# Kernel tuning notes

Measured on AMD Instinct MI355X. Metric: run time of the kernel, lower is better.

Reference implementation:

```python
import jax, jax.numpy as jnp
import numpy as np

B, T_IN, T_OUT, D, M, N = 4, 10, 5, 5, 96, 96
H1 = 64      # hidden dim of deep ConvLSTM layers
ATTN = 32    # attention bottleneck channels
SEL = 0      # selected_dim


def _conv(x, w, b):
    # SAME conv, NCHW / OIHW
    p = (w.shape[-1] - 1) // 2
    y = jax.lax.conv_general_dilated(x, w, (1, 1), [(p, p), (p, p)],
                                     dimension_numbers=('NCHW', 'OIHW', 'NCHW'))
    return y + b[None, :, None, None]


def _cell(xt, h, c, w, b):
    # standard ConvLSTM cell (no peephole): conv over concat(x, h) -> i,f,o,g
    z = _conv(jnp.concatenate([xt, h], axis=1), w, b)
    i, f, o, g = jnp.split(z, 4, axis=1)
    c = jax.nn.sigmoid(f) * c + jax.nn.sigmoid(i) * jnp.tanh(g)
    h = jax.nn.sigmoid(o) * jnp.tanh(c)
    return h, c


def setup_inputs() -> dict:
    key = jax.random.key(0)
    ks = jax.random.split(key, 12)
    w = lambda k, s: jax.random.normal(k, s, jnp.float32) * 0.05
    z = lambda n: jnp.zeros((n,), jnp.float32)
    return {
        'x': jax.random.normal(ks[0], (B, T_IN, D, M, N), jnp.float32),
        # encoder ConvLSTM cells: hidden dims [1, H1, H1]
        'enc_w0': w(ks[1], (4 * 1, D + 1, 3, 3)), 'enc_b0': z(4 * 1),
        'enc_w1': w(ks[2], (4 * H1, 1 + H1, 3, 3)), 'enc_b1': z(4 * H1),
        'enc_w2': w(ks[3], (4 * H1, H1 + H1, 3, 3)), 'enc_b2': z(4 * H1),
        # decoder ConvLSTM cells: hidden dims [H1, H1, 1]
        'dec_w0': w(ks[4], (4 * H1, 1 + H1, 3, 3)), 'dec_b0': z(4 * H1),
        'dec_w1': w(ks[5], (4 * H1, H1 + H1, 3, 3)), 'dec_b1': z(4 * H1),
        'dec_w2': w(ks[6], (4 * 1, H1 + 1, 3, 3)), 'dec_b2': z(4 * 1),
        # input attention (DA-RNN style with convs): e_k = v(tanh(Wi*x_k + Wh*[h;c]))
        'attn_wi': w(ks[7], (ATTN, T_IN, 3, 3)), 'attn_bi': z(ATTN),
        'attn_wh': w(ks[8], (ATTN, 2, 3, 3)), 'attn_bh': z(ATTN),
        'attn_wv': w(ks[9], (1, ATTN, 3, 3)), 'attn_bv': z(1),
        # temporal_cnn: Conv2d(1 + window_in, 1, kernel_size=1) + ReLU
        'tcnn_w': w(ks[10], (1, T_IN + 1, 1, 1)), 'tcnn_b': z(1),
    }


def reference(x, enc_w0, enc_b0, enc_w1, enc_b1, enc_w2, enc_b2,
              dec_w0, dec_b0, dec_w1, dec_b1, dec_w2, dec_b2,
              attn_wi, attn_bi, attn_wh, attn_bh, attn_wv, attn_bv,
              tcnn_w, tcnn_b):
    b = x.shape[0]

    def attn_reweight(xs, h, c):
        # xs: (b, t, d, m, n); hidden term shared across the d channels
        hid_e = _conv(jnp.concatenate([h, c], axis=1), attn_wh, attn_bh)
        def per_k(xk):  # (b, t, m, n): time-as-channels
            e = jnp.tanh(_conv(xk, attn_wi, attn_bi) + hid_e)
            return _conv(e, attn_wv, attn_bv)[:, 0]  # (b, m, n)
        alpha = jax.vmap(per_k, in_axes=2, out_axes=1)(xs)  # (b, d, m, n)
        ea = jnp.exp(alpha)
        return xs * (ea / jnp.max(ea))[:, None]  # global-max normalization

    def run_layer(xs, h, c, w, bb):
        def step(carry, xt):
            hh, cc = _cell(xt, carry[0], carry[1], w, bb)
            return (hh, cc), hh
        (h, c), hs = jax.lax.scan(step, (h, c), jnp.swapaxes(xs, 0, 1))
        return jnp.swapaxes(hs, 0, 1), (h, c)

    # ---------- encoder ----------
    h0 = jnp.zeros((b, 1, M, N), x.dtype); c0 = jnp.zeros_like(h0)
    def enc0_step(carry, t):
        xs, h, c = carry
        xs = attn_reweight(xs, h, c)  # re-weight whole sequence each step
        xt = jax.lax.dynamic_index_in_dim(xs, t, axis=1, keepdims=False)
        h, c = _cell(xt, h, c, enc_w0, enc_b0)
        return (xs, h, c), h
    (_, h0, c0), hs0 = jax.lax.scan(enc0_step, (x, h0, c0), jnp.arange(T_IN))
    out0 = jnp.swapaxes(hs0, 0, 1)  # (b, T_IN, 1, m, n)

    h1 = jnp.zeros((b, H1, M, N), x.dtype); c1 = jnp.zeros_like(h1)
    out1, (h1, c1) = run_layer(out0, h1, c1, enc_w1, enc_b1)
    h2 = jnp.zeros((b, H1, M, N), x.dtype); c2 = jnp.zeros_like(h2)
    out2, (h2, c2) = run_layer(out1, h2, c2, enc_w2, enc_b2)

    # ---------- decoder (encoder states reversed) ----------
    dec_in = jnp.zeros((b, T_OUT, 1, M, N), x.dtype)
    d0, _ = run_layer(dec_in, h2, c2, dec_w0, dec_b0)
    d1, _ = run_layer(d0, h1, c1, dec_w1, dec_b1)

    y_prev = x[:, :, SEL]  # (b, T_IN, m, n): selected variable, time-as-channels
    def dec2_step(carry, xt):
        h, c, yp = carry
        h, c = _cell(xt, h, c, dec_w2, dec_b2)          # (b, 1, m, n)
        ycat = jnp.concatenate([yp, h], axis=1)         # (b, T_IN+1, m, n)
        h = jax.nn.relu(_conv(ycat, tcnn_w, tcnn_b))    # temporal 1x1 CNN readout
        return (h, c, ycat[:, 1:]), h
    _, hs = jax.lax.scan(dec2_step, (h0, c0, y_prev), jnp.swapaxes(d1, 0, 1))
    return jnp.swapaxes(hs, 0, 1)  # (b, T_OUT, 1, m, n)
```

## Files before the change

kernel.cpp:

```cpp
#include <hip/hip_runtime.h>


#define PIX  9216
#define NB   4
#define TIN  10
#define TOUT 5
#define ND   5
#define HID  64

typedef __attribute__((ext_vector_type(8))) short bf16x8;
typedef __attribute__((ext_vector_type(4))) float f32x4;

__device__ __forceinline__ float sigmf_(float x) { return 1.0f / (1.0f + __expf(-x)); }
__device__ __forceinline__ float tanhf_(float x) { return 1.0f - 2.0f / (__expf(2.0f * x) + 1.0f); }
__device__ __forceinline__ unsigned short f2bf(float f) {
    unsigned u = __float_as_uint(f);
    unsigned r = u + 0x7FFFu + ((u >> 16) & 1u);
    return (unsigned short)(r >> 16);
}
__device__ __forceinline__ float bf2f(unsigned short u) {
    return __uint_as_float(((unsigned)u) << 16);
}
__device__ __forceinline__ unsigned fmap_(float f) {
    unsigned u = __float_as_uint(f);
    return (u & 0x80000000u) ? ~u : (u | 0x80000000u);
}
__device__ __forceinline__ float funmap_(unsigned v) {
    return __uint_as_float((v & 0x80000000u) ? (v ^ 0x80000000u) : ~v);
}
__device__ __forceinline__ void gload_lds16(const void* g, void* l) {
    __builtin_amdgcn_global_load_lds(
        (const __attribute__((address_space(1))) void*)g,
        (__attribute__((address_space(3))) void*)l, 16, 0, 0);
}

template <int NCH>
__device__ __forceinline__ void
cell64_body(char* smem, int bid,
            const unsigned short* __restrict__ inP,
            const unsigned short* __restrict__ wP,
            const float* __restrict__ bias,
            const float* cprev, float* cout,
            const float* __restrict__ zeropg,
            unsigned short* __restrict__ d1, int d1_coff, int d1_ncg,
            unsigned short* __restrict__ d2, int d2_coff, int d2_ncg)
{
    const int lane = threadIdx.x;
    const int wv   = threadIdx.y;
    const int tid  = wv * 64 + lane;
    const int rid = (bid & 7) * 48 + (bid >> 3);
    const int y = rid % 96, b = rid / 96;
    const int l15 = lane & 15, l4 = lane >> 4;
    const int NCG = NCH * 4;

    const int scg  = tid & 3;
    const int spr0 = tid >> 2;

    auto stage = [&](char* buf, int cc) {
#pragma unroll
        for (int i = 0; i < 5; ++i) {
            int pr = spr0 + i * 64;
            int r = pr / 98;
            int p = pr - r * 98;
            int gy = y - 1 + r, gx = p - 1;
            const void* g = (const void*)zeropg;
            if (pr < 294 && (unsigned)gy < 96u && (unsigned)gx < 96u) {
                int cg = scg ^ ((p >> 1) & 3);
                g = (const void*)(inP + (((size_t)(b * NCG + cc * 4 + cg) * 9216
                                          + gy * 96 + gx) << 3));
            }
            gload_lds16(g, buf + i * 4096 + wv * 1024);
        }
    };

    f32x4 acc[4][6] = {};
    bf16x8 af[3][4];

#pragma unroll
    for (int t0 = 0; t0 < 2; ++t0)
#pragma unroll
        for (int g = 0; g < 4; ++g)
            af[t0][g] = *(const bf16x8*)(wP
                + ((size_t)(t0 * NCH + 0) * 256 + g * 64 + wv * 16 + l15) * 32 + l4 * 8);

    stage(smem, 0);
    __syncthreads();
#pragma unroll
    for (int cc = 0; cc < NCH; ++cc) {
        if (cc + 1 < NCH) stage(smem + ((cc + 1) & 1) * 20480, cc + 1);
        const char* buf = smem + (cc & 1) * 20480;
#pragma unroll
        for (int tap = 0; tap < 9; ++tap) {
            const int T = cc * 9 + tap;
            const int Tp = T + 2;
            if (Tp < NCH * 9) {
                const int cc2 = Tp / 9, tap2 = Tp % 9;
#pragma unroll
                for (int g = 0; g < 4; ++g)
                    af[Tp % 3][g] = *(const bf16x8*)(wP
                        + ((size_t)(tap2 * NCH + cc2) * 256 + g * 64 + wv * 16 + l15) * 32 + l4 * 8);
            }
            const int ky = tap / 3, kx = tap % 3;
            bf16x8 bk[6];
#pragma unroll
            for (int k = 0; k < 6; ++k) {
                int p = k * 16 + kx + l15;
                int slot = l4 ^ ((p >> 1) & 3);
                bk[k] = *(const bf16x8*)(buf + (ky * 98 + p) * 64 + slot * 16);
            }
            __builtin_amdgcn_s_setprio(1);
#pragma unroll
            for (int g = 0; g < 4; ++g)
#pragma unroll
                for (int k = 0; k < 6; ++k)
                    acc[g][k] = __builtin_amdgcn_mfma_f32_16x16x32_bf16(
                        af[T % 3][g], bk[k], acc[g][k], 0, 0, 0);
            __builtin_amdgcn_s_setprio(0);
        }
        if (cc + 1 < NCH) __syncthreads();
    }

#pragma unroll
    for (int r = 0; r < 4; ++r) {
        int hc = wv * 16 + l4 * 4 + r;
        float bi = bias[hc], bff = bias[64 + hc];
        float bo = bias[128 + hc], bg = bias[192 + hc];
#pragma unroll
        for (int k = 0; k < 6; ++k) {
            int px = k * 16 + l15;
            int gpix = y * 96 + px;
            float ii = sigmf_(acc[0][k][r] + bi);
            float ff = sigmf_(acc[1][k][r] + bff);
            float oo = sigmf_(acc[2][k][r] + bo);
            float gg = tanhf_(acc[3][k][r] + bg);
            int cidx = (b * HID + hc) * 9216 + gpix;
            float cn = ff * cprev[cidx] + ii * gg;
            cout[cidx] = cn;
            unsigned short hb = f2bf(oo * tanhf_(cn));
            int ch1 = d1_coff + hc;
            d1[((size_t)(b * d1_ncg + (ch1 >> 3)) * 9216 + gpix) * 8 + (ch1 & 7)] = hb;
            if (d2) {
                int ch2 = d2_coff + hc;
                d2[((size_t)(b * d2_ncg + (ch2 >> 3)) * 9216 + gpix) * 8 + (ch2 & 7)] = hb;
            }
        }
    }
}

__device__ __forceinline__ void
attnE_body(char* smem, int aid,
           const unsigned short* __restrict__ xsp, const unsigned short* __restrict__ wiP,
           const float* __restrict__ h0, const float* __restrict__ c0,
           const float* __restrict__ wh, const float* __restrict__ bh,
           const float* __restrict__ bi, unsigned short* __restrict__ eP)
{
    float* heS = (float*)smem;
    const int lane = threadIdx.x, wvid = threadIdx.y;
    const int tile = aid % 36, k = (aid / 36) % 5, bb = aid / 180;
    const int l15 = lane & 15, l4 = lane >> 4;
    const int tid = wvid * 64 + lane;

    {
        int p = tile * 256 + tid;
        int y = p / 96, x = p - y * 96;
        float hv9[9], cv9[9];
        const float* hp = h0 + bb * PIX;
        const float* cp = c0 + bb * PIX;
#pragma unroll
        for (int t9 = 0; t9 < 9; ++t9) {
            int gy = y + t9 / 3 - 1, gx = x + t9 % 3 - 1;
            bool ok = (unsigned)gy < 96u && (unsigned)gx < 96u;
            hv9[t9] = ok ? hp[gy * 96 + gx] : 0.0f;
            cv9[t9] = ok ? cp[gy * 96 + gx] : 0.0f;
        }
#pragma unroll
        for (int ch = 0; ch < 32; ++ch) {
            float a = bi[ch] + bh[ch];
#pragma unroll
            for (int t9 = 0; t9 < 9; ++t9) {
                a = fmaf(wh[(ch * 2 + 0) * 9 + t9], hv9[t9], a);
                a = fmaf(wh[(ch * 2 + 1) * 9 + t9], cv9[t9], a);
            }
            heS[tid * 33 + ch] = a;
        }
    }

    bf16x8 af[5][2];
#pragma unroll
    for (int j = 0; j < 5; ++j)
#pragma unroll
        for (int m = 0; m < 2; ++m)
            af[j][m] = *(const bf16x8*)(wiP + ((size_t)(j * 32 + m * 16 + l15)) * 32 + l4 * 8);

    const unsigned short* xb = xsp + (size_t)(bb * ND + k) * PIX * 16;
    const int p0 = tile * 256 + wvid * 64;

    f32x4 acc[4][2] = {};
#pragma unroll
    for (int nf = 0; nf < 4; ++nf) {
        int p = p0 + nf * 16 + l15;
        int y = p / 96, x = p - y * 96;
#pragma unroll
        for (int j = 0; j < 5; ++j) {
            int tp = 2 * j + (l4 >> 1);
            bf16x8 bk = { 0, 0, 0, 0, 0, 0, 0, 0 };
            if (tp < 9) {
                int gy = y + tp / 3 - 1, gx = x + tp % 3 - 1;
                if ((unsigned)gy < 96u && (unsigned)gx < 96u)
                    bk = *(const bf16x8*)(xb + ((size_t)(gy * 96 + gx)) * 16 + (l4 & 1) * 8);
            }
            acc[nf][0] = __builtin_amdgcn_mfma_f32_16x16x32_bf16(af[j][0], bk, acc[nf][0], 0, 0, 0);
            acc[nf][1] = __builtin_amdgcn_mfma_f32_16x16x32_bf16(af[j][1], bk, acc[nf][1], 0, 0, 0);
        }
    }

    __syncthreads();

#pragma unroll
    for (int nf = 0; nf < 4; ++nf) {
        int p = p0 + nf * 16 + l15;
        int pl = wvid * 64 + nf * 16 + l15;
        const float* hrow = &heS[pl * 33];
#pragma unroll
        for (int m = 0; m < 2; ++m) {
            ushort4 o;
            o.x = f2bf(tanhf_(acc[nf][m][0] + hrow[m * 16 + l4 * 4 + 0]));
            o.y = f2bf(tanhf_(acc[nf][m][1] + hrow[m * 16 + l4 * 4 + 1]));
            o.z = f2bf(tanhf_(acc[nf][m][2] + hrow[m * 16 + l4 * 4 + 2]));
            o.w = f2bf(tanhf_(acc[nf][m][3] + hrow[m * 16 + l4 * 4 + 3]));
            *(ushort4*)(eP + ((size_t)(bb * ND + k) * PIX + p) * 32 + m * 16 + l4 * 4) = o;
        }
    }
}

__device__ __forceinline__ void
alpha_body(char* smem, int aid,
           const unsigned short* __restrict__ eP, const float* __restrict__ wvv,
           const float* __restrict__ bv, float* __restrict__ alpha,
           unsigned* __restrict__ msl)
{
    const int tid = threadIdx.y * 64 + threadIdx.x;
    const int tile = aid % 36, k = (aid / 36) % 5, bb = aid / 180;
    int p = tile * 256 + tid;
    int y = p / 96, x = p - y * 96;
    const unsigned short* eb = eP + (size_t)(bb * ND + k) * PIX * 32;
    float acc = bv[0];
#pragma unroll
    for (int ky = 0; ky < 3; ++ky) {
        int gy = y + ky - 1;
        if ((unsigned)gy >= 96u) continue;
#pragma unroll
        for (int kx = 0; kx < 3; ++kx) {
            int gx = x + kx - 1;
            if ((unsigned)gx >= 96u) continue;
            int tap = ky * 3 + kx;
            const unsigned short* ee = eb + ((size_t)(gy * 96 + gx)) * 32;
#pragma unroll
            for (int cg = 0; cg < 4; ++cg) {
                bf16x8 ev = *(const bf16x8*)(ee + cg * 8);
#pragma unroll
                for (int jj = 0; jj < 8; ++jj)
                    acc = fmaf(wvv[(cg * 8 + jj) * 9 + tap], bf2f((unsigned short)ev[jj]), acc);
            }
        }
    }
    alpha[(size_t)(bb * ND + k) * PIX + p] = acc;

    float* s = (float*)smem;
    s[tid] = acc;
    __syncthreads();
    for (int st = 128; st > 0; st >>= 1) {
        if (tid < st) s[tid] = fmaxf(s[tid], s[tid + st]);
        __syncthreads();
    }
    if (tid == 0) atomicMax(msl, fmap_(s[0]));
}

__device__ __forceinline__ void
dec2_body(int did,
          const unsigned short* __restrict__ inP, int ncg, int cgbase,
          const float* __restrict__ hprev, const float* cprev,
          const unsigned short* __restrict__ wm, const float* __restrict__ w2,
          const float* __restrict__ bias,
          const float* __restrict__ tw, const float* __restrict__ tb,
          const float* __restrict__ yprev,
          float* __restrict__ ynext, float* __restrict__ hcarry,
          float* __restrict__ outp, float* cout)
{
    const int wv = threadIdx.y, lane = threadIdx.x;
    const int l15 = lane & 15, l4 = lane >> 4;
    const int bx = did % 144, b = did / 144;
    const int p0 = (bx * 4 + wv) * 16;
    const int y = p0 / 96, xbase = p0 - y * 96;
    const int x = xbase + l15;

    f32x4 acc = {0.f, 0.f, 0.f, 0.f};
#pragma unroll
    for (int ky = 0; ky < 3; ++ky) {
        int gy = y + ky - 1;
        bool oky = (unsigned)gy < 96u;
#pragma unroll
        for (int kx = 0; kx < 3; ++kx) {
            const int tap = ky * 3 + kx;
            int gx = x + kx - 1;
            bool ok = oky && ((unsigned)gx < 96u);
#pragma unroll
            for (int cc = 0; cc < 2; ++cc) {
                bf16x8 a = *(const bf16x8*)(wm + ((size_t)(tap * 2 + cc) * 16 + l15) * 32 + l4 * 8);
                bf16x8 bk = { 0, 0, 0, 0, 0, 0, 0, 0 };
                if (ok)
                    bk = *(const bf16x8*)(inP + ((size_t)(b * ncg + cgbase + cc * 4 + l4) * 9216
                                                 + gy * 96 + gx) * 8);
                acc = __builtin_amdgcn_mfma_f32_16x16x32_bf16(a, bk, acc, 0, 0, 0);
            }
        }
    }

    if (l4 == 0) {
        int px = p0 + l15;
        float aI = acc[0] + bias[0];
        float aF = acc[1] + bias[1];
        float aO = acc[2] + bias[2];
        float aG = acc[3] + bias[3];
        const float* hp = hprev + b * PIX;
#pragma unroll
        for (int ky = 0; ky < 3; ++ky) {
            int gy = y + ky - 1;
            if ((unsigned)gy >= 96u) continue;
#pragma unroll
            for (int kx = 0; kx < 3; ++kx) {
                int gx = x + kx - 1;
                if ((unsigned)gx >= 96u) continue;
                int tap = ky * 3 + kx;
                float hv = hp[gy * 96 + gx];
                aI = fmaf(w2[(0 * 65 + 64) * 9 + tap], hv, aI);
                aF = fmaf(w2[(1 * 65 + 64) * 9 + tap], hv, aF);
                aO = fmaf(w2[(2 * 65 + 64) * 9 + tap], hv, aO);
                aG = fmaf(w2[(3 * 65 + 64) * 9 + tap], hv, aG);
            }
        }
        int idx = b * PIX + px;
        float cn = sigmf_(aF) * cprev[idx] + sigmf_(aI) * tanhf_(aG);
        cout[idx] = cn;
        float h = sigmf_(aO) * tanhf_(cn);

        float a2 = tb[0];
#pragma unroll
        for (int c2 = 0; c2 < TIN; ++c2)
            a2 = fmaf(tw[c2], yprev[(size_t)(b * TIN + c2) * PIX + px], a2);
        a2 = fmaf(tw[TIN], h, a2);
        float o = fmaxf(a2, 0.0f);
        outp[(size_t)b * TOUT * PIX + px] = o;
#pragma unroll
        for (int c2 = 0; c2 < TIN - 1; ++c2)
            ynext[(size_t)(b * TIN + c2) * PIX + px] = yprev[(size_t)(b * TIN + c2 + 1) * PIX + px];
        ynext[(size_t)(b * TIN + 9) * PIX + px] = h;
        hcarry[idx] = o;
    }
}

template <int NCH, bool ATTN>
__global__ void __launch_bounds__(256, 2)
mk_cell_attnE(const unsigned short* __restrict__ inP, const unsigned short* __restrict__ wP,
              const float* __restrict__ bias, const float* cprev, float* cout,
              const float* __restrict__ zeropg,
              unsigned short* __restrict__ d1, int d1_coff, int d1_ncg,
              unsigned short* __restrict__ d2, int d2_coff, int d2_ncg,
              const unsigned short* __restrict__ xsp, const unsigned short* __restrict__ wiP,
              const float* __restrict__ h0, const float* __restrict__ c0,
              const float* __restrict__ wh, const float* __restrict__ bh,
              const float* __restrict__ bi, unsigned short* __restrict__ eP)
{
    __shared__ __align__(16) char smem[40960];
    if (blockIdx.x < 384)
        cell64_body<NCH>(smem, blockIdx.x, inP, wP, bias, cprev, cout, zeropg,
                         d1, d1_coff, d1_ncg, d2, d2_coff, d2_ncg);
    else if (ATTN)
        attnE_body(smem, blockIdx.x - 384, xsp, wiP, h0, c0, wh, bh, bi, eP);
}

template <int NCH, bool ATTN>
__global__ void __launch_bounds__(256, 2)
mk_cell_alpha(const unsigned short* __restrict__ inP, const unsigned short* __restrict__ wP,
              const float* __restrict__ bias, const float* cprev, float* cout,
              const float* __restrict__ zeropg,
              unsigned short* __restrict__ d1, int d1_coff, int d1_ncg,
              unsigned short* __restrict__ d2, int d2_coff, int d2_ncg,
              const unsigned short* __restrict__ eP, const float* __restrict__ wvv,
              const float* __restrict__ bv, float* __restrict__ alpha,
              unsigned* __restrict__ msl)
{
    __shared__ __align__(16) char smem[40960];
    if (blockIdx.x < 384)
        cell64_body<NCH>(smem, blockIdx.x, inP, wP, bias, cprev, cout, zeropg,
                         d1, d1_coff, d1_ncg, d2, d2_coff, d2_ncg);
    else if (ATTN)
        alpha_body(smem, blockIdx.x - 384, eP, wvv, bv, alpha, msl);
}

__global__ void __launch_bounds__(256)
mk_scale_small5(const float* __restrict__ xs_cur, float* __restrict__ xs_nxt,
                unsigned short* __restrict__ xsp,
                const float* __restrict__ alpha, const unsigned* __restrict__ msl,
                int ts,
                const float* __restrict__ h0in, const float* cprev,
                const float* __restrict__ w, const float* __restrict__ bias,
                float* __restrict__ h0out, float* cout,
                unsigned short* __restrict__ pk, int ncg)
{
    __shared__ float z[4][64];
    const int bid = blockIdx.x;
    const float mval = funmap_(msl[0]);
    if (bid < 720) {
        int idx = bid * 256 + threadIdx.x;
        int p = idx % PIX;
        int q = idx / PIX;
        int d = q % ND, bb = q / ND;
        float wgt = __expf(alpha[idx] - mval);
        unsigned short tmp[16];
#pragma unroll
        for (int t = 0; t < TIN; ++t) {
            size_t xi = ((size_t)(bb * TIN + t) * ND + d) * PIX + p;
            float v = xs_cur[xi] * wgt;
            xs_nxt[xi] = v;
            tmp[t] = f2bf(v);
        }
#pragma unroll
        for (int t = TIN; t < 16; ++t) tmp[t] = 0;
        uint4* dst = (uint4*)(xsp + (size_t)idx * 16);
        dst[0] = *(uint4*)&tmp[0];
        dst[1] = *(uint4*)&tmp[8];
    } else {
        int bid2 = bid - 720;
        int bx = bid2 % 144, bb = bid2 / 144;
        const int pxl = threadIdx.x & 63, gate = threadIdx.x >> 6;
        const int p = bx * 64 + pxl;
        const int y = p / 96, x = p - y * 96;
        float acc = bias[gate];
#pragma unroll
        for (int cin = 0; cin < 6; ++cin) {
            const float* wp = w + (gate * 6 + cin) * 9;
#pragma unroll
            for (int ky = 0; ky < 3; ++ky) {
                int gy = y + ky - 1;
                if ((unsigned)gy >= 96u) continue;
#pragma unroll
                for (int kx = 0; kx < 3; ++kx) {
                    int gx = x + kx - 1;
                    if ((unsigned)gx >= 96u) continue;
                    int np = gy * 96 + gx;
                    float v;
                    if (cin < 5) {
                        float raw = xs_cur[((size_t)(bb * TIN + ts) * ND + cin) * PIX + np];
                        v = raw * __expf(alpha[(size_t)(bb * ND + cin) * PIX + np] - mval);
                    } else {
                        v = h0in[bb * PIX + np];
                    }
                    acc = fmaf(wp[ky * 3 + kx], v, acc);
                }
            }
        }
        z[gate][pxl] = acc;
        __syncthreads();
        if (threadIdx.x < 64) {
            int pp = bx * 64 + threadIdx.x;
            int idx = bb * PIX + pp;
            float cn = sigmf_(z[1][threadIdx.x]) * cprev[idx]
                     + sigmf_(z[0][threadIdx.x]) * tanhf_(z[3][threadIdx.x]);
            cout[idx] = cn;
            float h = sigmf_(z[2][threadIdx.x]) * tanhf_(cn);
            h0out[idx] = h;
            pk[((size_t)(bb * ncg) * 9216 + pp) * 8] = f2bf(h);
        }
    }
}

template <bool HAS0, bool HAS2>
__global__ void __launch_bounds__(256, 2)
mk_dec(const unsigned short* __restrict__ d1in, const unsigned short* __restrict__ wpd1,
       const float* __restrict__ b1, float* c1, unsigned short* __restrict__ d1out,
       const float* __restrict__ zeropg,
       const unsigned short* __restrict__ d0in, const unsigned short* __restrict__ wpd0,
       const float* __restrict__ b0, float* c2, unsigned short* __restrict__ d0out,
       unsigned short* __restrict__ d1next,
       const unsigned short* __restrict__ d2in,
       const float* __restrict__ hprev, float* c0,
       const unsigned short* __restrict__ wd2m, const float* __restrict__ w2,
       const float* __restrict__ b2,
       const float* __restrict__ tw, const float* __restrict__ tb,
       const float* __restrict__ yprev, float* __restrict__ ynext,
       float* __restrict__ hcarry, float* __restrict__ outp)
{
    __shared__ __align__(16) char smem[40960];
    if (blockIdx.x < 384) {
        cell64_body<4>(smem, blockIdx.x, d1in, wpd1, b1, c1, c1, zeropg,
                       d1out, 64, 16, nullptr, 0, 0);
    } else if (blockIdx.x < 768) {
        if (HAS0)
            cell64_body<2>(smem, blockIdx.x - 384, d0in, wpd0, b0, c2, c2, zeropg,
                           d0out, 0, 8, d1next, 0, 16);
    } else {
        if (HAS2)
            dec2_body(blockIdx.x - 768, d2in, 16, 8, hprev, c0, wd2m, w2, b2,
                      tw, tb, yprev, ynext, hcarry, outp, c0);
    }
}

template <int NCH>
__global__ void __launch_bounds__(256, 2)
cell_k(const unsigned short* __restrict__ inP, const unsigned short* __restrict__ wP,
       const float* __restrict__ bias, const float* cprev, float* cout,
       const float* __restrict__ zeropg,
       unsigned short* __restrict__ d1, int d1_coff, int d1_ncg,
       unsigned short* __restrict__ d2, int d2_coff, int d2_ncg)
{
    __shared__ __align__(16) char smem[40960];
    cell64_body<NCH>(smem, blockIdx.x, inP, wP, bias, cprev, cout, zeropg,
                     d1, d1_coff, d1_ncg, d2, d2_coff, d2_ncg);
}

__global__ void __launch_bounds__(256)
dec2_k(const unsigned short* __restrict__ d2in, const float* __restrict__ hprev,
       float* c0, const unsigned short* __restrict__ wd2m, const float* __restrict__ w2,
       const float* __restrict__ b2, const float* __restrict__ tw, const float* __restrict__ tb,
       const float* __restrict__ yprev, float* __restrict__ ynext,
       float* __restrict__ hcarry, float* __restrict__ outp)
{
    dec2_body(blockIdx.x, d2in, 16, 8, hprev, c0, wd2m, w2, b2,
              tw, tb, yprev, ynext, hcarry, outp, c0);
}

__global__ void __launch_bounds__(256)
attn_e_k(const unsigned short* __restrict__ xsp, const unsigned short* __restrict__ wiP,
         const float* __restrict__ h0, const float* __restrict__ c0,
         const float* __restrict__ wh, const float* __restrict__ bh,
         const float* __restrict__ bi, unsigned short* __restrict__ eP)
{
    __shared__ __align__(16) char smem[33792];
    attnE_body(smem, blockIdx.x, xsp, wiP, h0, c0, wh, bh, bi, eP);
}

__global__ void __launch_bounds__(256)
alpha_k(const unsigned short* __restrict__ eP, const float* __restrict__ wvv,
        const float* __restrict__ bv, float* __restrict__ alpha, unsigned* __restrict__ msl)
{
    __shared__ __align__(16) char smem[1024];
    alpha_body(smem, blockIdx.x, eP, wvv, bv, alpha, msl);
}

__global__ void __launch_bounds__(256)
prep_kernel(const float* __restrict__ enc_w1, const float* __restrict__ enc_w2,
            const float* __restrict__ dec_w0, const float* __restrict__ dec_w1,
            const float* __restrict__ dec_w2, const float* __restrict__ attn_wi,
            const float* __restrict__ x,
            unsigned short* __restrict__ wpe1, unsigned short* __restrict__ wpe2,
            unsigned short* __restrict__ wpd0, unsigned short* __restrict__ wpd1,
            unsigned short* __restrict__ wd2m, unsigned short* __restrict__ wiP,
            unsigned short* __restrict__ xsp, float* __restrict__ yp)
{
    int gid = blockIdx.x;
    auto wpack = [&](const float* w, unsigned short* wp, int WCIN, int NCH,
                     int coff, int climit, int base) {
        int idx = (gid - base) * 256 + threadIdx.x;
        if (idx >= 9 * NCH * 256 * 32) return;
        int k = idx & 31;
        int ocp = (idx >> 5) & 255;
        int rest = idx >> 13;
        int cc = rest % NCH, tap = rest / NCH;
        int hc = ocp >> 2, gate = ocp & 3;
        int c = cc * 32 + k;
        float v = 0.0f;
        if (c < climit) v = w[((gate * 64 + hc) * WCIN + (c + coff)) * 9 + tap];
        wp[idx] = f2bf(v);
    };
    if (gid < 864) { wpack(enc_w1, wpe1, 65, 3, 0, 65, 0); return; }
    if (gid < 2016) { wpack(enc_w2, wpe2, 128, 4, 0, 128, 864); return; }
    if (gid < 2592) { wpack(dec_w0, wpd0, 65, 2, 1, 64, 2016); return; }
    if (gid < 3744) { wpack(dec_w1, wpd1, 128, 4, 0, 128, 2592); return; }
    if (gid < 3780) {
        int idx = (gid - 3744) * 256 + threadIdx.x;
        if (idx < 9 * 2 * 16 * 32) {
            int k = idx & 31;
            int oc = (idx >> 5) & 15;
            int cc = (idx >> 9) & 1;
            int tap = idx >> 10;
            float v = 0.0f;
            if (oc < 4) v = dec_w2[(oc * 65 + cc * 32 + k) * 9 + tap];
            wd2m[idx] = f2bf(v);
        }
        return;
    }
    if (gid < 3800) {
        int idx = (gid - 3780) * 256 + threadIdx.x;
        if (idx < 5120) {
            int kl = idx & 31, oc = (idx >> 5) & 31, j = idx >> 10;
            int tappos = kl >> 4, ch = kl & 15;
            int tap = 2 * j + tappos;
            float v = 0.0f;
            if (tap < 9 && ch < 10) v = attn_wi[(oc * TIN + ch) * 9 + tap];
            wiP[idx] = f2bf(v);
        }
        return;
    }
    if (gid < 4520) {
        int idx = (gid - 3800) * 256 + threadIdx.x;
        int p = idx % PIX;
        int q = idx / PIX;
        int d = q % ND, bb = q / ND;
        unsigned short tmp[16];
#pragma unroll
        for (int t = 0; t < TIN; ++t)
            tmp[t] = f2bf(x[((size_t)(bb * TIN + t) * ND + d) * PIX + p]);
#pragma unroll
        for (int t = TIN; t < 16; ++t) tmp[t] = 0;
        uint4* dst = (uint4*)(xsp + (size_t)idx * 16);
        dst[0] = *(uint4*)&tmp[0];
        dst[1] = *(uint4*)&tmp[8];
        return;
    }
    {
        int idx = (gid - 4520) * 256 + threadIdx.x;
        int p = idx % PIX;
        int q = idx / PIX;
        yp[idx] = x[(size_t)(q * ND + 0) * PIX + p];
    }
}

extern "C" void kernel_launch(void* const* d_in, const int* in_sizes, int n_in,
                              void* d_out, int out_size, void* d_ws, size_t ws_size,
                              hipStream_t stream)
{
    const float* x       = (const float*)d_in[0];
    const float* enc_w0  = (const float*)d_in[1];
    const float* enc_b0  = (const float*)d_in[2];
    const float* enc_w1  = (const float*)d_in[3];
    const float* enc_b1  = (const float*)d_in[4];
    const float* enc_w2  = (const float*)d_in[5];
    const float* enc_b2  = (const float*)d_in[6];
    const float* dec_w0  = (const float*)d_in[7];
    const float* dec_b0  = (const float*)d_in[8];
    const float* dec_w1  = (const float*)d_in[9];
    const float* dec_b1  = (const float*)d_in[10];
    const float* dec_w2  = (const float*)d_in[11];
    const float* dec_b2  = (const float*)d_in[12];
    const float* attn_wi = (const float*)d_in[13];
    const float* attn_bi = (const float*)d_in[14];
    const float* attn_wh = (const float*)d_in[15];
    const float* attn_bh = (const float*)d_in[16];
    const float* attn_wv = (const float*)d_in[17];
    const float* attn_bv = (const float*)d_in[18];
    const float* tcnn_w  = (const float*)d_in[19];
    const float* tcnn_b  = (const float*)d_in[20];
    float* out = (float*)d_out;

    char* cur = (char*)d_ws;
    auto alloc = [&](size_t bytes) { char* p = cur; cur += (bytes + 255) & ~(size_t)255; return p; };
    float* xsA  = (float*)alloc((size_t)NB * TIN * ND * PIX * 4);
    float* xsB  = (float*)alloc((size_t)NB * TIN * ND * PIX * 4);
    float* alp  = (float*)alloc((size_t)NB * ND * PIX * 4);
    float* ypa  = (float*)alloc((size_t)NB * TIN * PIX * 4);
    float* ypb  = (float*)alloc((size_t)NB * TIN * PIX * 4);
    unsigned short* wpe1 = (unsigned short*)alloc((size_t)9 * 3 * 256 * 32 * 2);
    unsigned short* wpe2 = (unsigned short*)alloc((size_t)9 * 4 * 256 * 32 * 2);
    unsigned short* wpd0 = (unsigned short*)alloc((size_t)9 * 2 * 256 * 32 * 2);
    unsigned short* wpd1 = (unsigned short*)alloc((size_t)9 * 4 * 256 * 32 * 2);
    unsigned short* wd2m = (unsigned short*)alloc((size_t)9 * 2 * 16 * 32 * 2);
    unsigned short* xsp  = (unsigned short*)alloc((size_t)NB * ND * PIX * 16 * 2);
    unsigned short* wiP  = (unsigned short*)alloc(5120 * 2);
    unsigned short* eP   = (unsigned short*)alloc((size_t)NB * ND * PIX * 32 * 2);
    char* zbeg = cur;
    float* h0a  = (float*)alloc(NB * PIX * 4);
    float* h0b  = (float*)alloc(NB * PIX * 4);
    float* c0   = (float*)alloc(NB * PIX * 4);
    float* c1   = (float*)alloc((size_t)NB * HID * PIX * 4);
    float* c2   = (float*)alloc((size_t)NB * HID * PIX * 4);
    const size_t IN1_B = (size_t)NB * 12 * PIX * 8 * 2;
    const size_t IN2_B = (size_t)NB * 16 * PIX * 8 * 2;
    unsigned short* In1a = (unsigned short*)alloc(IN1_B);
    unsigned short* In1b = (unsigned short*)alloc(IN1_B);
    unsigned short* In2a = (unsigned short*)alloc(IN2_B);
    unsigned short* In2b = (unsigned short*)alloc(IN2_B);
    unsigned* mslot = (unsigned*)alloc(256);
    float* zeropg = (float*)alloc(256);
    char* zend = cur;

    hipMemcpyAsync(xsA, x, (size_t)NB * TIN * ND * PIX * 4, hipMemcpyDeviceToDevice, stream);
    hipMemsetAsync(zbeg, 0, (size_t)(zend - zbeg), stream);
    prep_kernel<<<dim3(5960), 256, 0, stream>>>(enc_w1, enc_w2, dec_w0, dec_w1, dec_w2,
                                                attn_wi, x, wpe1, wpe2, wpd0, wpd1,
                                                wd2m, wiP, xsp, ypa);

    dim3 blk(64, 4);
    float *h0 = h0a, *h0n = h0b;
    float *xc = xsA, *xn = xsB;
    unsigned short *i1c = In1a, *i1n = In1b, *i2c = In2a, *i2n = In2b;

    attn_e_k<<<dim3(720), blk, 0, stream>>>(xsp, wiP, h0, c0, attn_wh, attn_bh, attn_bi, eP);
    alpha_k<<<dim3(720), blk, 0, stream>>>(eP, attn_wv, attn_bv, alp, mslot + 0);
    mk_scale_small5<<<dim3(1296), 256, 0, stream>>>(xc, xn, xsp, alp, mslot + 0, 0,
                                                    h0, c0, enc_w0, enc_b0, h0n, c0, i1c, 12);
    { float* tmp = h0; h0 = h0n; h0n = tmp; }
    { float* tmp = xc; xc = xn; xn = tmp; }

    for (int t = 0; t < TIN; ++t) {
        const bool hn = (t < TIN - 1);
        unsigned short* e1d1 = hn ? i1n : In2a;
        int e1o = hn ? 1 : 64;
        int e1n = hn ? 12 : 16;
        unsigned short* e2d1 = hn ? i2n : In1a;
        int e2o = hn ? 64 : 0;
        int e2n = hn ? 16 : 8;
        int grid = 384 + (hn ? 720 : 0);

        if (hn)
            mk_cell_attnE<3, true><<<dim3(grid), blk, 0, stream>>>(
                i1c, wpe1, enc_b1, c1, c1, zeropg, e1d1, e1o, e1n, i2c, 0, 16,
                xsp, wiP, h0, c0, attn_wh, attn_bh, attn_bi, eP);
        else
            mk_cell_attnE<3, false><<<dim3(grid), blk, 0, stream>>>(
                i1c, wpe1, enc_b1, c1, c1, zeropg, e1d1, e1o, e1n, i2c, 0, 16,
                xsp, wiP, h0, c0, attn_wh, attn_bh, attn_bi, eP);

        if (hn)
            mk_cell_alpha<4, true><<<dim3(grid), blk, 0, stream>>>(
                i2c, wpe2, enc_b2, c2, c2, zeropg, e2d1, e2o, e2n, nullptr, 0, 0,
                eP, attn_wv, attn_bv, alp, mslot + t + 1);
        else
            mk_cell_alpha<4, false><<<dim3(grid), blk, 0, stream>>>(
                i2c, wpe2, enc_b2, c2, c2, zeropg, e2d1, e2o, e2n, nullptr, 0, 0,
                eP, attn_wv, attn_bv, alp, mslot + t + 1);

        if (hn) {
            mk_scale_small5<<<dim3(1296), 256, 0, stream>>>(xc, xn, xsp, alp, mslot + t + 1,
                                                            t + 1, h0, c0, enc_w0, enc_b0,
                                                            h0n, c0, i1n, 12);
            { float* tmp = h0; h0 = h0n; h0n = tmp; }
            { float* tmp = xc; xc = xn; xn = tmp; }
        }
        { unsigned short* tmp = i1c; i1c = i1n; i1n = tmp; }
        { unsigned short* tmp = i2c; i2c = i2n; i2n = tmp; }
    }

    float *hc = h0, *hcn = h0n;
    cell_k<2><<<dim3(384), blk, 0, stream>>>(In1a, wpd0, dec_b0, c2, c2, zeropg,
                                             In1b, 0, 8, In2a, 0, 16);
    mk_dec<true, false><<<dim3(768), blk, 0, stream>>>(
        In2a, wpd1, dec_b1, c1, In2b, zeropg,
        In1b, wpd0, dec_b0, c2, In1a, In2b,
        nullptr, nullptr, nullptr, nullptr, nullptr, nullptr, nullptr, nullptr,
        nullptr, nullptr, nullptr, nullptr);
    mk_dec<true, true><<<dim3(1344), blk, 0, stream>>>(
        In2b, wpd1, dec_b1, c1, In2a, zeropg,
        In1a, wpd0, dec_b0, c2, In1b, In2a,
        In2b, hc, c0, wd2m, dec_w2, dec_b2, tcnn_w, tcnn_b,
        ypa, ypb, hcn, out + 0 * PIX);
    mk_dec<true, true><<<dim3(1344), blk, 0, stream>>>(
        In2a, wpd1, dec_b1, c1, In2b, zeropg,
        In1b, wpd0, dec_b0, c2, In1a, In2b,
        In2a, hcn, c0, wd2m, dec_w2, dec_b2, tcnn_w, tcnn_b,
        ypb, ypa, hc, out + 1 * PIX);
    mk_dec<true, true><<<dim3(1344), blk, 0, stream>>>(
        In2b, wpd1, dec_b1, c1, In2a, zeropg,
        In1a, wpd0, dec_b0, c2, In1b, In2a,
        In2b, hc, c0, wd2m, dec_w2, dec_b2, tcnn_w, tcnn_b,
        ypa, ypb, hcn, out + 2 * PIX);
    mk_dec<false, true><<<dim3(1344), blk, 0, stream>>>(
        In2a, wpd1, dec_b1, c1, In2b, zeropg,
        nullptr, nullptr, nullptr, nullptr, nullptr, nullptr,
        In2a, hcn, c0, wd2m, dec_w2, dec_b2, tcnn_w, tcnn_b,
        ypb, ypa, hc, out + 3 * PIX);
    dec2_k<<<dim3(576), blk, 0, stream>>>(In2b, hc, c0, wd2m, dec_w2, dec_b2,
                                          tcnn_w, tcnn_b, ypa, ypb, hcn, out + 4 * PIX);
}
```

Baseline: 1.270 ms.

## Split encoder layer-1 single input channel into separate direct-gather MFMA pass

The encoder layer-1 cell previously packed its one input channel plus 64 hidden channels into 3 channel chunks (65 channels padded to 96). The input channel is now handled by a dedicated MFMA pass that gathers the 9 conv taps of the fp32 h0 map directly from global memory, using a separately packed weight slice. This lets the main loop run over only 2 chunks, and the scale kernel no longer writes h0 into the packed bf16 input buffer. It removes a mostly-padding chunk of LDS staging and MFMA work, at the cost of uncoalesced scalar global gathers and extra registers in the cell kernel.

```diff
diff --git a/kernel.cpp b/kernel.cpp
--- a/kernel.cpp
+++ b/kernel.cpp
@@ -34,7 +34,7 @@
         (__attribute__((address_space(3))) void*)l, 16, 0, 0);
 }
 
-template <int NCH>
+template <int NCH, bool XCONV>
 __device__ __forceinline__ void
 cell64_body(char* smem, int bid,
             const unsigned short* __restrict__ inP,
@@ -43,7 +43,8 @@
             const float* cprev, float* cout,
             const float* __restrict__ zeropg,
             unsigned short* __restrict__ d1, int d1_coff, int d1_ncg,
-            unsigned short* __restrict__ d2, int d2_coff, int d2_ncg)
+            unsigned short* __restrict__ d2, int d2_coff, int d2_ncg,
+            const float* __restrict__ xim, const unsigned short* __restrict__ wxP)
 {
     const int lane = threadIdx.x;
     const int wv   = threadIdx.y;
@@ -118,6 +119,33 @@
             __builtin_amdgcn_s_setprio(0);
         }
         if (cc + 1 < NCH) __syncthreads();
+    }
+
+    if (XCONV) {
+        bf16x8 afx[4];
+#pragma unroll
+        for (int g = 0; g < 4; ++g)
+            afx[g] = *(const bf16x8*)(wxP
+                + ((size_t)(g * 64 + wv * 16 + l15)) * 32 + l4 * 8);
+        const float* xb = xim + b * PIX;
+#pragma unroll
+        for (int k = 0; k < 6; ++k) {
+            int p = k * 16 + l15;
+            bf16x8 bx = { 0, 0, 0, 0, 0, 0, 0, 0 };
+#pragma unroll
+            for (int j = 0; j < 8; ++j) {
+                int tap = l4 * 8 + j;
+                if (tap < 9) {
+                    int gy = y + tap / 3 - 1, gx = p + tap % 3 - 1;
+                    if ((unsigned)gy < 96u && (unsigned)gx < 96u)
+                        bx[j] = (short)f2bf(xb[gy * 96 + gx]);
+                }
+            }
+#pragma unroll
+            for (int g = 0; g < 4; ++g)
+                acc[g][k] = __builtin_amdgcn_mfma_f32_16x16x32_bf16(
+                    afx[g], bx, acc[g][k], 0, 0, 0);
+        }
     }
 
 #pragma unroll
@@ -359,13 +387,14 @@
     }
 }
 
-template <int NCH, bool ATTN>
+template <int NCH, bool XCONV, bool ATTN>
 __global__ void __launch_bounds__(256, 2)
 mk_cell_attnE(const unsigned short* __restrict__ inP, const unsigned short* __restrict__ wP,
               const float* __restrict__ bias, const float* cprev, float* cout,
               const float* __restrict__ zeropg,
               unsigned short* __restrict__ d1, int d1_coff, int d1_ncg,
               unsigned short* __restrict__ d2, int d2_coff, int d2_ncg,
+              const float* __restrict__ xim, const unsigned short* __restrict__ wxP,
               const unsigned short* __restrict__ xsp, const unsigned short* __restrict__ wiP,
               const float* __restrict__ h0, const float* __restrict__ c0,
               const float* __restrict__ wh, const float* __restrict__ bh,
@@ -373,8 +402,8 @@
 {
     __shared__ __align__(16) char smem[40960];
     if (blockIdx.x < 384)
-        cell64_body<NCH>(smem, blockIdx.x, inP, wP, bias, cprev, cout, zeropg,
-                         d1, d1_coff, d1_ncg, d2, d2_coff, d2_ncg);
+        cell64_body<NCH, XCONV>(smem, blockIdx.x, inP, wP, bias, cprev, cout, zeropg,
+                                d1, d1_coff, d1_ncg, d2, d2_coff, d2_ncg, xim, wxP);
     else if (ATTN)
         attnE_body(smem, blockIdx.x - 384, xsp, wiP, h0, c0, wh, bh, bi, eP);
 }
@@ -392,8 +421,8 @@
 {
     __shared__ __align__(16) char smem[40960];
     if (blockIdx.x < 384)
-        cell64_body<NCH>(smem, blockIdx.x, inP, wP, bias, cprev, cout, zeropg,
-                         d1, d1_coff, d1_ncg, d2, d2_coff, d2_ncg);
+        cell64_body<NCH, false>(smem, blockIdx.x, inP, wP, bias, cprev, cout, zeropg,
+                                d1, d1_coff, d1_ncg, d2, d2_coff, d2_ncg, nullptr, nullptr);
     else if (ATTN)
         alpha_body(smem, blockIdx.x - 384, eP, wvv, bv, alpha, msl);
 }
@@ -405,8 +434,7 @@
                 int ts,
                 const float* __restrict__ h0in, const float* cprev,
                 const float* __restrict__ w, const float* __restrict__ bias,
-                float* __restrict__ h0out, float* cout,
-                unsigned short* __restrict__ pk, int ncg)
+                float* __restrict__ h0out, float* cout)
 {
     __shared__ float z[4][64];
     const int bid = blockIdx.x;
@@ -468,9 +496,7 @@
             float cn = sigmf_(z[1][threadIdx.x]) * cprev[idx]
                      + sigmf_(z[0][threadIdx.x]) * tanhf_(z[3][threadIdx.x]);
             cout[idx] = cn;
-            float h = sigmf_(z[2][threadIdx.x]) * tanhf_(cn);
-            h0out[idx] = h;
-            pk[((size_t)(bb * ncg) * 9216 + pp) * 8] = f2bf(h);
+            h0out[idx] = sigmf_(z[2][threadIdx.x]) * tanhf_(cn);
         }
     }
 }
@@ -493,12 +519,12 @@
 {
     __shared__ __align__(16) char smem[40960];
     if (blockIdx.x < 384) {
-        cell64_body<4>(smem, blockIdx.x, d1in, wpd1, b1, c1, c1, zeropg,
-                       d1out, 64, 16, nullptr, 0, 0);
+        cell64_body<4, false>(smem, blockIdx.x, d1in, wpd1, b1, c1, c1, zeropg,
+                              d1out, 64, 16, nullptr, 0, 0, nullptr, nullptr);
     } else if (blockIdx.x < 768) {
         if (HAS0)
-            cell64_body<2>(smem, blockIdx.x - 384, d0in, wpd0, b0, c2, c2, zeropg,
-                           d0out, 0, 8, d1next, 0, 16);
+            cell64_body<2, false>(smem, blockIdx.x - 384, d0in, wpd0, b0, c2, c2, zeropg,
+                                  d0out, 0, 8, d1next, 0, 16, nullptr, nullptr);
     } else {
         if (HAS2)
             dec2_body(blockIdx.x - 768, d2in, 16, 8, hprev, c0, wd2m, w2, b2,
@@ -515,8 +541,8 @@
        unsigned short* __restrict__ d2, int d2_coff, int d2_ncg)
 {
     __shared__ __align__(16) char smem[40960];
-    cell64_body<NCH>(smem, blockIdx.x, inP, wP, bias, cprev, cout, zeropg,
-                     d1, d1_coff, d1_ncg, d2, d2_coff, d2_ncg);
+    cell64_body<NCH, false>(smem, blockIdx.x, inP, wP, bias, cprev, cout, zeropg,
+                            d1, d1_coff, d1_ncg, d2, d2_coff, d2_ncg, nullptr, nullptr);
 }
 
 __global__ void __launch_bounds__(256)
@@ -556,6 +582,7 @@
             unsigned short* __restrict__ wpe1, unsigned short* __restrict__ wpe2,
             unsigned short* __restrict__ wpd0, unsigned short* __restrict__ wpd1,
             unsigned short* __restrict__ wd2m, unsigned short* __restrict__ wiP,
+            unsigned short* __restrict__ wxP,
             unsigned short* __restrict__ xsp, float* __restrict__ yp)
 {
     int gid = blockIdx.x;
@@ -573,12 +600,12 @@
         if (c < climit) v = w[((gate * 64 + hc) * WCIN + (c + coff)) * 9 + tap];
         wp[idx] = f2bf(v);
     };
-    if (gid < 864) { wpack(enc_w1, wpe1, 65, 3, 0, 65, 0); return; }
-    if (gid < 2016) { wpack(enc_w2, wpe2, 128, 4, 0, 128, 864); return; }
-    if (gid < 2592) { wpack(dec_w0, wpd0, 65, 2, 1, 64, 2016); return; }
-    if (gid < 3744) { wpack(dec_w1, wpd1, 128, 4, 0, 128, 2592); return; }
-    if (gid < 3780) {
-        int idx = (gid - 3744) * 256 + threadIdx.x;
+    if (gid < 576) { wpack(enc_w1, wpe1, 65, 2, 1, 64, 0); return; }
+    if (gid < 1728) { wpack(enc_w2, wpe2, 128, 4, 0, 128, 576); return; }
+    if (gid < 2304) { wpack(dec_w0, wpd0, 65, 2, 1, 64, 1728); return; }
+    if (gid < 3456) { wpack(dec_w1, wpd1, 128, 4, 0, 128, 2304); return; }
+    if (gid < 3492) {
+        int idx = (gid - 3456) * 256 + threadIdx.x;
         if (idx < 9 * 2 * 16 * 32) {
             int k = idx & 31;
             int oc = (idx >> 5) & 15;
@@ -590,8 +617,8 @@
         }
         return;
     }
-    if (gid < 3800) {
-        int idx = (gid - 3780) * 256 + threadIdx.x;
+    if (gid < 3512) {
+        int idx = (gid - 3492) * 256 + threadIdx.x;
         if (idx < 5120) {
             int kl = idx & 31, oc = (idx >> 5) & 31, j = idx >> 10;
             int tappos = kl >> 4, ch = kl & 15;
@@ -602,8 +629,20 @@
         }
         return;
     }
-    if (gid < 4520) {
-        int idx = (gid - 3800) * 256 + threadIdx.x;
+    if (gid < 3544) {
+        int idx = (gid - 3512) * 256 + threadIdx.x;
+        if (idx < 8192) {
+            int s = idx & 31;
+            int ocp = idx >> 5;
+            int hc = ocp >> 2, gate = ocp & 3;
+            float v = 0.0f;
+            if (s < 9) v = enc_w1[((gate * 64 + hc) * 65 + 0) * 9 + s];
+            wxP[idx] = f2bf(v);
+        }
+        return;
+    }
+    if (gid < 4264) {
+        int idx = (gid - 3544) * 256 + threadIdx.x;
         int p = idx % PIX;
         int q = idx / PIX;
         int d = q % ND, bb = q / ND;
@@ -619,7 +658,7 @@
         return;
     }
     {
-        int idx = (gid - 4520) * 256 + threadIdx.x;
+        int idx = (gid - 4264) * 256 + threadIdx.x;
         int p = idx % PIX;
         int q = idx / PIX;
         yp[idx] = x[(size_t)(q * ND + 0) * PIX + p];
@@ -660,13 +699,14 @@
     float* alp  = (float*)alloc((size_t)NB * ND * PIX * 4);
     float* ypa  = (float*)alloc((size_t)NB * TIN * PIX * 4);
     float* ypb  = (float*)alloc((size_t)NB * TIN * PIX * 4);
-    unsigned short* wpe1 = (unsigned short*)alloc((size_t)9 * 3 * 256 * 32 * 2);
+    unsigned short* wpe1 = (unsigned short*)alloc((size_t)9 * 2 * 256 * 32 * 2);
     unsigned short* wpe2 = (unsigned short*)alloc((size_t)9 * 4 * 256 * 32 * 2);
     unsigned short* wpd0 = (unsigned short*)alloc((size_t)9 * 2 * 256 * 32 * 2);
     unsigned short* wpd1 = (unsigned short*)alloc((size_t)9 * 4 * 256 * 32 * 2);
     unsigned short* wd2m = (unsigned short*)alloc((size_t)9 * 2 * 16 * 32 * 2);
+    unsigned short* wiP  = (unsigned short*)alloc(5120 * 2);
+    unsigned short* wxP  = (unsigned short*)alloc(8192 * 2);
     unsigned short* xsp  = (unsigned short*)alloc((size_t)NB * ND * PIX * 16 * 2);
-    unsigned short* wiP  = (unsigned short*)alloc(5120 * 2);
     unsigned short* eP   = (unsigned short*)alloc((size_t)NB * ND * PIX * 32 * 2);
     char* zbeg = cur;
     float* h0a  = (float*)alloc(NB * PIX * 4);
@@ -674,7 +714,7 @@
     float* c0   = (float*)alloc(NB * PIX * 4);
     float* c1   = (float*)alloc((size_t)NB * HID * PIX * 4);
     float* c2   = (float*)alloc((size_t)NB * HID * PIX * 4);
-    const size_t IN1_B = (size_t)NB * 12 * PIX * 8 * 2;
+    const size_t IN1_B = (size_t)NB * 8 * PIX * 8 * 2;
     const size_t IN2_B = (size_t)NB * 16 * PIX * 8 * 2;
     unsigned short* In1a = (unsigned short*)alloc(IN1_B);
     unsigned short* In1b = (unsigned short*)alloc(IN1_B);
@@ -686,9 +726,9 @@
 
     hipMemcpyAsync(xsA, x, (size_t)NB * TIN * ND * PIX * 4, hipMemcpyDeviceToDevice, stream);
     hipMemsetAsync(zbeg, 0, (size_t)(zend - zbeg), stream);
-    prep_kernel<<<dim3(5960), 256, 0, stream>>>(enc_w1, enc_w2, dec_w0, dec_w1, dec_w2,
+    prep_kernel<<<dim3(5704), 256, 0, stream>>>(enc_w1, enc_w2, dec_w0, dec_w1, dec_w2,
                                                 attn_wi, x, wpe1, wpe2, wpd0, wpd1,
-                                                wd2m, wiP, xsp, ypa);
+                                                wd2m, wiP, wxP, xsp, ypa);
 
     dim3 blk(64, 4);
     float *h0 = h0a, *h0n = h0b;
@@ -698,27 +738,29 @@
     attn_e_k<<<dim3(720), blk, 0, stream>>>(xsp, wiP, h0, c0, attn_wh, attn_bh, attn_bi, eP);
     alpha_k<<<dim3(720), blk, 0, stream>>>(eP, attn_wv, attn_bv, alp, mslot + 0);
     mk_scale_small5<<<dim3(1296), 256, 0, stream>>>(xc, xn, xsp, alp, mslot + 0, 0,
-                                                    h0, c0, enc_w0, enc_b0, h0n, c0, i1c, 12);
+                                                    h0, c0, enc_w0, enc_b0, h0n, c0);
     { float* tmp = h0; h0 = h0n; h0n = tmp; }
     { float* tmp = xc; xc = xn; xn = tmp; }
 
     for (int t = 0; t < TIN; ++t) {
         const bool hn = (t < TIN - 1);
         unsigned short* e1d1 = hn ? i1n : In2a;
-        int e1o = hn ? 1 : 64;
-        int e1n = hn ? 12 : 16;
+        int e1o = hn ? 0 : 64;
+        int e1n = hn ? 8 : 16;
         unsigned short* e2d1 = hn ? i2n : In1a;
         int e2o = hn ? 64 : 0;
         int e2n = hn ? 16 : 8;
         int grid = 384 + (hn ? 720 : 0);
 
         if (hn)
-            mk_cell_attnE<3, true><<<dim3(grid), blk, 0, stream>>>(
+            mk_cell_attnE<2, true, true><<<dim3(grid), blk, 0, stream>>>(
                 i1c, wpe1, enc_b1, c1, c1, zeropg, e1d1, e1o, e1n, i2c, 0, 16,
+                h0, wxP,
                 xsp, wiP, h0, c0, attn_wh, attn_bh, attn_bi, eP);
         else
-            mk_cell_attnE<3, false><<<dim3(grid), blk, 0, stream>>>(
+            mk_cell_attnE<2, true, false><<<dim3(grid), blk, 0, stream>>>(
                 i1c, wpe1, enc_b1, c1, c1, zeropg, e1d1, e1o, e1n, i2c, 0, 16,
+                h0, wxP,
                 xsp, wiP, h0, c0, attn_wh, attn_bh, attn_bi, eP);
 
         if (hn)
@@ -733,7 +775,7 @@
         if (hn) {
             mk_scale_small5<<<dim3(1296), 256, 0, stream>>>(xc, xn, xsp, alp, mslot + t + 1,
                                                             t + 1, h0, c0, enc_w0, enc_b0,
-                                                            h0n, c0, i1n, 12);
+                                                            h0n, c0);
             { float* tmp = h0; h0 = h0n; h0n = tmp; }
             { float* tmp = xc; xc = xn; xn = tmp; }
         }
```

Result: no change. 1.280 ms (+0.8%).
